# Kernel tuning notes

Hardware: AMD Instinct MI355X
Metric: run time of the kernel (lower is better)

Reference implementation:

```python
import jax, jax.numpy as jnp
import numpy as np

N_NODES = 100000
N_EDGES = 800000
FEATURE_DIM = 128
DEPTH = 3


def setup_inputs() -> dict:
    key = jax.random.key(0)
    k1, k2, k3 = jax.random.split(key, 3)
    x = jax.random.normal(k1, (N_NODES, FEATURE_DIM), dtype=jnp.float32)
    edge_index = jax.random.randint(k2, (2, N_EDGES), 0, N_NODES, dtype=jnp.int32)
    W = jax.random.normal(k3, (FEATURE_DIM, FEATURE_DIM), dtype=jnp.float32) * (1.0 / np.sqrt(FEATURE_DIM))
    b = jnp.zeros((FEATURE_DIM,), dtype=jnp.float32)
    return {"x": x, "edge_index": edge_index, "W": W, "b": b}


def reference(x, edge_index, W, b):
    n = x.shape[0]
    # PyG GCNConv default: add self-loops, symmetric normalization
    loop = jnp.arange(n, dtype=edge_index.dtype)
    src = jnp.concatenate([edge_index[0], loop])  # [E+N]
    dst = jnp.concatenate([edge_index[1], loop])  # [E+N]
    ones = jnp.ones(src.shape[0], dtype=x.dtype)
    deg = jax.ops.segment_sum(ones, dst, num_segments=n)  # in-degree incl. self-loop
    dis = jnp.where(deg > 0, jax.lax.rsqrt(deg), 0.0)  # deg^{-1/2}
    norm = (dis[src] * dis[dst])[:, None]  # [E+N, 1]

    # depth iterations share the SAME conv weights (time-invariant)
    for _ in range(DEPTH):
        h = x @ W  # [N, D] linear transform first (PyG order)
        msg = h[src] * norm  # gather + normalize, [E+N, D]
        agg = jax.ops.segment_sum(msg, dst, num_segments=n)  # scatter-add
        x = jax.nn.relu(agg + b)  # bias, NullControl adds 0, dropout_rate=0 is identity
    return x
```

## Files before the change

kernel.cpp:

```cpp
#include <hip/hip_runtime.h>

#define FD 128

typedef __attribute__((ext_vector_type(8))) short short8;
typedef __attribute__((ext_vector_type(4))) float floatx4;

__device__ inline unsigned short f2bf(float f) {
  unsigned u = __float_as_uint(f);
  u += 0x7fffu + ((u >> 16) & 1u);
  return (unsigned short)(u >> 16);
}
__device__ inline float bf2f(unsigned short s) {
  return __uint_as_float(((unsigned)s) << 16);
}
__device__ inline float lo16f(unsigned v) { return __uint_as_float(v << 16); }
__device__ inline float hi16f(unsigned v) { return __uint_as_float(v & 0xffff0000u); }
__device__ inline int imin(int a, int b) { return a < b ? a : b; }


__global__ __launch_bounds__(256) void k_count(const int* __restrict__ dst,
                                               int* __restrict__ deg, int E) {
  int e = blockIdx.x * 256 + threadIdx.x;
  if (e < E) atomicAdd(&deg[dst[e]], 1);
}

__global__ __launch_bounds__(256) void k_scanA(const int* __restrict__ deg,
                                               int* __restrict__ offtmp,
                                               int* __restrict__ bsum,
                                               float* __restrict__ dis, int N) {
  __shared__ int s[256];
  int i = blockIdx.x * 256 + threadIdx.x;
  int v = (i < N) ? deg[i] : 0;
  if (i < N) dis[i] = rsqrtf((float)(v + 1));
  s[threadIdx.x] = v;
  __syncthreads();
#pragma unroll
  for (int ofs = 1; ofs < 256; ofs <<= 1) {
    int t = (threadIdx.x >= ofs) ? s[threadIdx.x - ofs] : 0;
    __syncthreads();
    s[threadIdx.x] += t;
    __syncthreads();
  }
  if (i < N) offtmp[i] = s[threadIdx.x] - v;
  if (threadIdx.x == 255) bsum[blockIdx.x] = s[255];
}

__global__ __launch_bounds__(512) void k_scanB(int* __restrict__ bsum, int nb) {
  __shared__ int s[512];
  int t = threadIdx.x;
  int v = (t < nb) ? bsum[t] : 0;
  s[t] = v;
  __syncthreads();
#pragma unroll
  for (int ofs = 1; ofs < 512; ofs <<= 1) {
    int u = (t >= ofs) ? s[t - ofs] : 0;
    __syncthreads();
    s[t] += u;
    __syncthreads();
  }
  if (t < nb) bsum[t] = s[t] - v;
}

__global__ __launch_bounds__(256) void k_scanC(const int* __restrict__ offtmp,
                                               const int* __restrict__ bsum,
                                               int* __restrict__ off, int N, int E) {
  int i = blockIdx.x * 256 + threadIdx.x;
  if (i < N) off[i] = offtmp[i] + bsum[i >> 8];
  if (i == 0) off[N] = E;
}

__global__ __launch_bounds__(256) void k_fill(const int* __restrict__ src,
                                              const int* __restrict__ dst,
                                              const float* __restrict__ dis,
                                              const int* __restrict__ off,
                                              int* __restrict__ cursor,
                                              int2* __restrict__ ew, int E) {
  int e = blockIdx.x * 256 + threadIdx.x;
  if (e >= E) return;
  int d = dst[e], s = src[e];
  int pos = off[d] + atomicAdd(&cursor[d], 1);
  ew[pos] = make_int2(s, __float_as_int(dis[s] * dis[d]));
}

__global__ __launch_bounds__(256) void k_wsplit(const float* __restrict__ W,
                                                short* __restrict__ hi,
                                                short* __restrict__ lo) {
  int idx = blockIdx.x * 256 + threadIdx.x;
  int j = idx & 7, lane = (idx >> 3) & 63, kt = (idx >> 9) & 3, ct = idx >> 11;
  int k = kt * 32 + (lane >> 4) * 8 + j;
  int n = ct * 16 + (lane & 15);
  float w = W[k * FD + n];
  unsigned short h = f2bf(w);
  hi[idx] = (short)h;
  lo[idx] = (short)f2bf(w - bf2f(h));
}

template <bool ABF16, bool WLO>
__global__ __launch_bounds__(256) void k_gemm(const void* __restrict__ Av,
                                              const short* __restrict__ Wf_hi,
                                              const short* __restrict__ Wf_lo,
                                              unsigned short* __restrict__ H, int N) {
  __shared__ short whi[FD * FD];
  __shared__ short wlo[WLO ? FD * FD : 8];
  int tid = threadIdx.x;
#pragma unroll
  for (int it = 0; it < 8; ++it) {
    int idx = (it * 256 + tid) * 8;
    *(short8*)&whi[idx] = *(const short8*)&Wf_hi[idx];
    if (WLO) *(short8*)&wlo[idx] = *(const short8*)&Wf_lo[idx];
  }
  __syncthreads();

  int wid = tid >> 6, lane = tid & 63;
  int quad = lane >> 4, m = lane & 15;
  int rbase = blockIdx.x * 128 + wid * 32;

  short8 ahi[2][4], alo[2][4];
#pragma unroll
  for (int t = 0; t < 2; ++t) {
    int arow = rbase + t * 16 + m;
    if (arow >= N) arow = N - 1;
    if (ABF16) {
      const unsigned short* ap = (const unsigned short*)Av + (size_t)arow * FD;
#pragma unroll
      for (int kt = 0; kt < 4; ++kt)
        ahi[t][kt] = *(const short8*)(ap + kt * 32 + quad * 8);
    } else {
      const float* ap = (const float*)Av + (size_t)arow * FD;
#pragma unroll
      for (int kt = 0; kt < 4; ++kt) {
        const float* p = ap + kt * 32 + quad * 8;
        float4 a0 = *(const float4*)p;
        float4 a1 = *(const float4*)(p + 4);
        float av[8] = {a0.x, a0.y, a0.z, a0.w, a1.x, a1.y, a1.z, a1.w};
#pragma unroll
        for (int j = 0; j < 8; ++j) {
          unsigned short hb = f2bf(av[j]);
          ahi[t][kt][j] = (short)hb;
          alo[t][kt][j] = (short)f2bf(av[j] - bf2f(hb));
        }
      }
    }
  }

#pragma unroll
  for (int ct = 0; ct < 8; ++ct) {
    floatx4 acc0 = {0.f, 0.f, 0.f, 0.f}, acc1 = {0.f, 0.f, 0.f, 0.f};
#pragma unroll
    for (int kt = 0; kt < 4; ++kt) {
      int fo = (((ct << 2) + kt) * 64 + lane) * 8;
      short8 bhi = *(const short8*)&whi[fo];
      acc0 = __builtin_amdgcn_mfma_f32_16x16x32_bf16(ahi[0][kt], bhi, acc0, 0, 0, 0);
      acc1 = __builtin_amdgcn_mfma_f32_16x16x32_bf16(ahi[1][kt], bhi, acc1, 0, 0, 0);
      if (!ABF16) {
        acc0 = __builtin_amdgcn_mfma_f32_16x16x32_bf16(alo[0][kt], bhi, acc0, 0, 0, 0);
        acc1 = __builtin_amdgcn_mfma_f32_16x16x32_bf16(alo[1][kt], bhi, acc1, 0, 0, 0);
      }
      if (WLO) {
        short8 blo = *(const short8*)&wlo[fo];
        acc0 = __builtin_amdgcn_mfma_f32_16x16x32_bf16(ahi[0][kt], blo, acc0, 0, 0, 0);
        acc1 = __builtin_amdgcn_mfma_f32_16x16x32_bf16(ahi[1][kt], blo, acc1, 0, 0, 0);
      }
    }
#pragma unroll
    for (int r = 0; r < 4; ++r) {
      int row0 = rbase + quad * 4 + r;
      int row1 = rbase + 16 + quad * 4 + r;
      if (row0 < N) H[(size_t)row0 * FD + ct * 16 + m] = f2bf(acc0[r]);
      if (row1 < N) H[(size_t)row1 * FD + ct * 16 + m] = f2bf(acc1[r]);
    }
  }
}

template <bool OUTBF16>
__global__ __launch_bounds__(256) void k_agg(const unsigned int* __restrict__ h,
                                             const int* __restrict__ off,
                                             const int2* __restrict__ ew,
                                             const float* __restrict__ dis,
                                             const float* __restrict__ bias,
                                             void* __restrict__ out, int N) {
  int lane = threadIdx.x & 63;
  int i0 = __builtin_amdgcn_readfirstlane((blockIdx.x * 4 + (threadIdx.x >> 6)) * 4);
  if (i0 >= N) return;

  int b0 = off[i0];
  int b1 = off[imin(i0 + 1, N)];
  int b2 = off[imin(i0 + 2, N)];
  int b3 = off[imin(i0 + 3, N)];
  int b4 = off[imin(i0 + 4, N)];

  float ax[4], ay[4];
#pragma unroll
  for (int t = 0; t < 4; ++t) {
    int i = i0 + t;
    if (i < N) {
      float di = dis[i];
      float ws = di * di;
      unsigned v = h[(size_t)i * 64 + lane];
      ax[t] = ws * lo16f(v);
      ay[t] = ws * hi16f(v);
    } else {
      ax[t] = 0.f;
      ay[t] = 0.f;
    }
  }

  int p = b0, pe = b4;
  if (p < pe) {
    int2 e0[4], e1[4];
    unsigned g0[4];
#pragma unroll
    for (int j = 0; j < 4; ++j) e0[j] = ew[imin(p + j, pe - 1)];
#pragma unroll
    for (int j = 0; j < 4; ++j) g0[j] = h[(size_t)e0[j].x * 64 + lane];
#pragma unroll
    for (int j = 0; j < 4; ++j) e1[j] = ew[imin(p + 4 + j, pe - 1)];

    for (int q = p; q < pe; q += 4) {
      unsigned g1[4];
      int2 e2[4];
#pragma unroll
      for (int j = 0; j < 4; ++j) g1[j] = h[(size_t)e1[j].x * 64 + lane];
#pragma unroll
      for (int j = 0; j < 4; ++j) e2[j] = ew[imin(q + 8 + j, pe - 1)];
#pragma unroll
      for (int j = 0; j < 4; ++j) {
        int qq = q + j;
        if (qq < pe) {
          float w = __int_as_float(e0[j].y);
          float l = lo16f(g0[j]), hh = hi16f(g0[j]);
          if (qq < b1) {
            ax[0] = fmaf(w, l, ax[0]); ay[0] = fmaf(w, hh, ay[0]);
          } else if (qq < b2) {
            ax[1] = fmaf(w, l, ax[1]); ay[1] = fmaf(w, hh, ay[1]);
          } else if (qq < b3) {
            ax[2] = fmaf(w, l, ax[2]); ay[2] = fmaf(w, hh, ay[2]);
          } else {
            ax[3] = fmaf(w, l, ax[3]); ay[3] = fmaf(w, hh, ay[3]);
          }
        }
      }
#pragma unroll
      for (int j = 0; j < 4; ++j) { e0[j] = e1[j]; e1[j] = e2[j]; g0[j] = g1[j]; }
    }
  }

  float2 bb = ((const float2*)bias)[lane];
#pragma unroll
  for (int t = 0; t < 4; ++t) {
    int i = i0 + t;
    if (i < N) {
      float o0 = fmaxf(ax[t] + bb.x, 0.f);
      float o1 = fmaxf(ay[t] + bb.y, 0.f);
      if (OUTBF16) {
        unsigned pk = ((unsigned)f2bf(o1) << 16) | (unsigned)f2bf(o0);
        ((unsigned*)out)[(size_t)i * 64 + lane] = pk;
      } else {
        ((float2*)out)[(size_t)i * 64 + lane] = make_float2(o0, o1);
      }
    }
  }
}


extern "C" void kernel_launch(void* const* d_in, const int* in_sizes, int n_in,
                              void* d_out, int out_size, void* d_ws, size_t ws_size,
                              hipStream_t stream) {
  const float* x = (const float*)d_in[0];
  const int* ei = (const int*)d_in[1];
  const float* Wg = (const float*)d_in[2];
  const float* b = (const float*)d_in[3];
  int N = in_sizes[0] / FD;
  int E = in_sizes[1] / 2;
  const int* src = ei;
  const int* dst = ei + E;

  char* p = (char*)d_ws;
  auto alloc = [&](size_t bytes) {
    void* r = (void*)p;
    p += (bytes + 255) & ~(size_t)255;
    return r;
  };
  int* deg = (int*)alloc((size_t)N * 4);
  int* cursor = (int*)alloc((size_t)N * 4);
  float* dis = (float*)alloc((size_t)N * 4);
  int* offtmp = (int*)alloc((size_t)N * 4);
  int nb = (N + 255) / 256;
  int* bsum = (int*)alloc((size_t)nb * 4);
  int* off = (int*)alloc((size_t)(N + 1) * 4);
  int2* ew = (int2*)alloc((size_t)E * 8);
  unsigned short* h = (unsigned short*)alloc((size_t)N * FD * 2);
  unsigned short* xb = (unsigned short*)alloc((size_t)N * FD * 2);
  short* wf_hi = (short*)alloc((size_t)FD * FD * 2);
  short* wf_lo = (short*)alloc((size_t)FD * FD * 2);

  hipMemsetAsync(deg, 0, (size_t)N * 4, stream);
  hipMemsetAsync(cursor, 0, (size_t)N * 4, stream);

  int gE = (E + 255) / 256, gN = (N + 255) / 256;
  k_count<<<gE, 256, 0, stream>>>(dst, deg, E);
  k_scanA<<<nb, 256, 0, stream>>>(deg, offtmp, bsum, dis, N);
  k_scanB<<<1, 512, 0, stream>>>(bsum, nb);
  k_scanC<<<gN, 256, 0, stream>>>(offtmp, bsum, off, N, E);
  k_fill<<<gE, 256, 0, stream>>>(src, dst, dis, off, cursor, ew, E);
  k_wsplit<<<FD * FD / 256, 256, 0, stream>>>(Wg, wf_hi, wf_lo);

  int gG = (N + 127) / 128;
  int gA = (N + 15) / 16;
  k_gemm<false, true><<<gG, 256, 0, stream>>>(x, wf_hi, wf_lo, h, N);
  k_agg<true><<<gA, 256, 0, stream>>>((const unsigned*)h, off, ew, dis, b, xb, N);
  k_gemm<true, false><<<gG, 256, 0, stream>>>(xb, wf_hi, wf_lo, h, N);
  k_agg<true><<<gA, 256, 0, stream>>>((const unsigned*)h, off, ew, dis, b, xb, N);
  k_gemm<true, false><<<gG, 256, 0, stream>>>(xb, wf_hi, wf_lo, h, N);
  k_agg<false><<<gA, 256, 0, stream>>>((const unsigned*)h, off, ew, dis, b, d_out, N);
}
```

Measured before the change: 361.8 us.

## Fuse degree count into first GEMM launch and use one wave per node in aggregation

The degree-counting atomics now run in extra blocks of the first GEMM kernel, and weight splitting moves before it, so one launch and one memset disappear and the two kinds of work overlap. The aggregation kernel changes from one wave handling four nodes with branchy accumulator selection to one wave per node. That wave keeps 8 gathers in flight per iteration and spreads them over four independent accumulator pairs. The cost is more waves, some wasted gathers on low-degree nodes, and a larger shared-memory footprint in the fused GEMM kernel, which also holds the counting blocks.

Result: slower. 431.5 us (+19.2%).

```diff
diff --git a/kernel.cpp b/kernel.cpp
--- a/kernel.cpp
+++ b/kernel.cpp
@@ -17,12 +17,6 @@
 __device__ inline float hi16f(unsigned v) { return __uint_as_float(v & 0xffff0000u); }
 __device__ inline int imin(int a, int b) { return a < b ? a : b; }
 
-
-__global__ __launch_bounds__(256) void k_count(const int* __restrict__ dst,
-                                               int* __restrict__ deg, int E) {
-  int e = blockIdx.x * 256 + threadIdx.x;
-  if (e < E) atomicAdd(&deg[dst[e]], 1);
-}
 
 __global__ __launch_bounds__(256) void k_scanA(const int* __restrict__ deg,
                                                int* __restrict__ offtmp,
@@ -96,12 +90,11 @@
 }
 
 template <bool ABF16, bool WLO>
-__global__ __launch_bounds__(256) void k_gemm(const void* __restrict__ Av,
-                                              const short* __restrict__ Wf_hi,
-                                              const short* __restrict__ Wf_lo,
-                                              unsigned short* __restrict__ H, int N) {
-  __shared__ short whi[FD * FD];
-  __shared__ short wlo[WLO ? FD * FD : 8];
+__device__ __forceinline__ void gemm_body(const void* __restrict__ Av,
+                                          const short* __restrict__ Wf_hi,
+                                          const short* __restrict__ Wf_lo,
+                                          unsigned short* __restrict__ H, int N,
+                                          int blk, short* whi, short* wlo) {
   int tid = threadIdx.x;
 #pragma unroll
   for (int it = 0; it < 8; ++it) {
@@ -113,7 +106,7 @@
 
   int wid = tid >> 6, lane = tid & 63;
   int quad = lane >> 4, m = lane & 15;
-  int rbase = blockIdx.x * 128 + wid * 32;
+  int rbase = blk * 128 + wid * 32;
 
   short8 ahi[2][4], alo[2][4];
 #pragma unroll
@@ -172,6 +165,30 @@
   }
 }
 
+__global__ __launch_bounds__(256) void k_gemm_b(const unsigned short* __restrict__ A,
+                                                const short* __restrict__ Wf_hi,
+                                                unsigned short* __restrict__ H, int N) {
+  __shared__ short whi[FD * FD];
+  gemm_body<true, false>(A, Wf_hi, nullptr, H, N, blockIdx.x, whi, nullptr);
+}
+
+__global__ __launch_bounds__(256) void k_gemm0_count(const float* __restrict__ A,
+                                                     const short* __restrict__ Wf_hi,
+                                                     const short* __restrict__ Wf_lo,
+                                                     unsigned short* __restrict__ H, int N,
+                                                     int gemmBlocks,
+                                                     const int* __restrict__ dst,
+                                                     int* __restrict__ deg, int E) {
+  __shared__ short whi[FD * FD];
+  __shared__ short wlo[FD * FD];
+  if ((int)blockIdx.x < gemmBlocks) {
+    gemm_body<false, true>(A, Wf_hi, Wf_lo, H, N, blockIdx.x, whi, wlo);
+  } else {
+    int e = ((int)blockIdx.x - gemmBlocks) * 256 + threadIdx.x;
+    if (e < E) atomicAdd(&deg[dst[e]], 1);
+  }
+}
+
 template <bool OUTBF16>
 __global__ __launch_bounds__(256) void k_agg(const unsigned int* __restrict__ h,
                                              const int* __restrict__ off,
@@ -180,85 +197,49 @@
                                              const float* __restrict__ bias,
                                              void* __restrict__ out, int N) {
   int lane = threadIdx.x & 63;
-  int i0 = __builtin_amdgcn_readfirstlane((blockIdx.x * 4 + (threadIdx.x >> 6)) * 4);
-  if (i0 >= N) return;
-
-  int b0 = off[i0];
-  int b1 = off[imin(i0 + 1, N)];
-  int b2 = off[imin(i0 + 2, N)];
-  int b3 = off[imin(i0 + 3, N)];
-  int b4 = off[imin(i0 + 4, N)];
-
-  float ax[4], ay[4];
-#pragma unroll
-  for (int t = 0; t < 4; ++t) {
-    int i = i0 + t;
-    if (i < N) {
-      float di = dis[i];
-      float ws = di * di;
-      unsigned v = h[(size_t)i * 64 + lane];
-      ax[t] = ws * lo16f(v);
-      ay[t] = ws * hi16f(v);
-    } else {
-      ax[t] = 0.f;
-      ay[t] = 0.f;
-    }
-  }
-
-  int p = b0, pe = b4;
-  if (p < pe) {
-    int2 e0[4], e1[4];
-    unsigned g0[4];
-#pragma unroll
-    for (int j = 0; j < 4; ++j) e0[j] = ew[imin(p + j, pe - 1)];
-#pragma unroll
-    for (int j = 0; j < 4; ++j) g0[j] = h[(size_t)e0[j].x * 64 + lane];
-#pragma unroll
-    for (int j = 0; j < 4; ++j) e1[j] = ew[imin(p + 4 + j, pe - 1)];
-
-    for (int q = p; q < pe; q += 4) {
-      unsigned g1[4];
-      int2 e2[4];
-#pragma unroll
-      for (int j = 0; j < 4; ++j) g1[j] = h[(size_t)e1[j].x * 64 + lane];
-#pragma unroll
-      for (int j = 0; j < 4; ++j) e2[j] = ew[imin(q + 8 + j, pe - 1)];
-#pragma unroll
-      for (int j = 0; j < 4; ++j) {
-        int qq = q + j;
-        if (qq < pe) {
-          float w = __int_as_float(e0[j].y);
-          float l = lo16f(g0[j]), hh = hi16f(g0[j]);
-          if (qq < b1) {
-            ax[0] = fmaf(w, l, ax[0]); ay[0] = fmaf(w, hh, ay[0]);
-          } else if (qq < b2) {
-            ax[1] = fmaf(w, l, ax[1]); ay[1] = fmaf(w, hh, ay[1]);
-          } else if (qq < b3) {
-            ax[2] = fmaf(w, l, ax[2]); ay[2] = fmaf(w, hh, ay[2]);
-          } else {
-            ax[3] = fmaf(w, l, ax[3]); ay[3] = fmaf(w, hh, ay[3]);
-          }
-        }
-      }
-#pragma unroll
-      for (int j = 0; j < 4; ++j) { e0[j] = e1[j]; e1[j] = e2[j]; g0[j] = g1[j]; }
+  int i = blockIdx.x * 4 + (threadIdx.x >> 6);
+  if (i >= N) return;
+  int p0 = off[i], p1 = off[i + 1];
+  float di = dis[i];
+  float ws = di * di;
+  unsigned v = h[(size_t)i * 64 + lane];
+  float a0 = ws * lo16f(v), a1 = ws * hi16f(v);
+  float b0 = 0.f, b1 = 0.f, c0 = 0.f, c1 = 0.f, d0 = 0.f, d1 = 0.f;
+
+  if (p0 < p1) {
+    int pe1 = p1 - 1;
+    int2 eb[8];
+#pragma unroll
+    for (int j = 0; j < 8; ++j) eb[j] = ew[imin(p0 + j, pe1)];
+    for (int p = p0; p < p1; p += 8) {
+      unsigned g[8];
+#pragma unroll
+      for (int j = 0; j < 8; ++j) g[j] = h[(size_t)eb[j].x * 64 + lane];
+      int2 enx[8];
+#pragma unroll
+      for (int j = 0; j < 8; ++j) enx[j] = ew[imin(p + 8 + j, pe1)];
+#pragma unroll
+      for (int j = 0; j < 8; ++j) {
+        float w = (p + j < p1) ? __int_as_float(eb[j].y) : 0.f;
+        float l = lo16f(g[j]), hh = hi16f(g[j]);
+        if (j == 0 || j == 4) { a0 = fmaf(w, l, a0); a1 = fmaf(w, hh, a1); }
+        else if (j == 1 || j == 5) { b0 = fmaf(w, l, b0); b1 = fmaf(w, hh, b1); }
+        else if (j == 2 || j == 6) { c0 = fmaf(w, l, c0); c1 = fmaf(w, hh, c1); }
+        else { d0 = fmaf(w, l, d0); d1 = fmaf(w, hh, d1); }
+      }
+#pragma unroll
+      for (int j = 0; j < 8; ++j) eb[j] = enx[j];
     }
   }
 
   float2 bb = ((const float2*)bias)[lane];
-#pragma unroll
-  for (int t = 0; t < 4; ++t) {
-    int i = i0 + t;
-    if (i < N) {
-      float o0 = fmaxf(ax[t] + bb.x, 0.f);
-      float o1 = fmaxf(ay[t] + bb.y, 0.f);
-      if (OUTBF16) {
-        unsigned pk = ((unsigned)f2bf(o1) << 16) | (unsigned)f2bf(o0);
-        ((unsigned*)out)[(size_t)i * 64 + lane] = pk;
-      } else {
-        ((float2*)out)[(size_t)i * 64 + lane] = make_float2(o0, o1);
-      }
-    }
+  float o0 = fmaxf((a0 + b0) + (c0 + d0) + bb.x, 0.f);
+  float o1 = fmaxf((a1 + b1) + (c1 + d1) + bb.y, 0.f);
+  if (OUTBF16) {
+    unsigned pk = ((unsigned)f2bf(o1) << 16) | (unsigned)f2bf(o0);
+    ((unsigned*)out)[(size_t)i * 64 + lane] = pk;
+  } else {
+    ((float2*)out)[(size_t)i * 64 + lane] = make_float2(o0, o1);
   }
 }
 
@@ -281,8 +262,8 @@
     p += (bytes + 255) & ~(size_t)255;
     return r;
   };
-  int* deg = (int*)alloc((size_t)N * 4);
-  int* cursor = (int*)alloc((size_t)N * 4);
+  int* deg = (int*)alloc((size_t)N * 8);
+  int* cursor = deg + N;
   float* dis = (float*)alloc((size_t)N * 4);
   int* offtmp = (int*)alloc((size_t)N * 4);
   int nb = (N + 255) / 256;
@@ -294,23 +275,22 @@
   short* wf_hi = (short*)alloc((size_t)FD * FD * 2);
   short* wf_lo = (short*)alloc((size_t)FD * FD * 2);
 
-  hipMemsetAsync(deg, 0, (size_t)N * 4, stream);
-  hipMemsetAsync(cursor, 0, (size_t)N * 4, stream);
+  hipMemsetAsync(deg, 0, (size_t)N * 8, stream);
 
   int gE = (E + 255) / 256, gN = (N + 255) / 256;
-  k_count<<<gE, 256, 0, stream>>>(dst, deg, E);
+  int gG = (N + 127) / 128;
+  int gA = (N + 3) / 4;
+
+  k_wsplit<<<FD * FD / 256, 256, 0, stream>>>(Wg, wf_hi, wf_lo);
+  k_gemm0_count<<<gG + gE, 256, 0, stream>>>(x, wf_hi, wf_lo, h, N, gG, dst, deg, E);
   k_scanA<<<nb, 256, 0, stream>>>(deg, offtmp, bsum, dis, N);
   k_scanB<<<1, 512, 0, stream>>>(bsum, nb);
   k_scanC<<<gN, 256, 0, stream>>>(offtmp, bsum, off, N, E);
   k_fill<<<gE, 256, 0, stream>>>(src, dst, dis, off, cursor, ew, E);
-  k_wsplit<<<FD * FD / 256, 256, 0, stream>>>(Wg, wf_hi, wf_lo);
-
-  int gG = (N + 127) / 128;
-  int gA = (N + 15) / 16;
-  k_gemm<false, true><<<gG, 256, 0, stream>>>(x, wf_hi, wf_lo, h, N);
+
   k_agg<true><<<gA, 256, 0, stream>>>((const unsigned*)h, off, ew, dis, b, xb, N);
-  k_gemm<true, false><<<gG, 256, 0, stream>>>(xb, wf_hi, wf_lo, h, N);
+  k_gemm_b<<<gG, 256, 0, stream>>>(xb, wf_hi, h, N);
   k_agg<true><<<gA, 256, 0, stream>>>((const unsigned*)h, off, ew, dis, b, xb, N);
-  k_gemm<true, false><<<gG, 256, 0, stream>>>(xb, wf_hi, wf_lo, h, N);
+  k_gemm_b<<<gG, 256, 0, stream>>>(xb, wf_hi, h, N);
   k_agg<false><<<gA, 256, 0, stream>>>((const unsigned*)h, off, ew, dis, b, d_out, N);
 }
```
